# Optimization experiments

Measured on AMD Instinct MI355X. Metric: run time of the kernel, lower is better.

Reference implementation:

```python
import jax, jax.numpy as jnp
import numpy as np

N, C, H, W = 16, 512, 32, 32
NH = 8            # num_heads
HD = C // NH      # head dim c = 64
G = C // 4        # GroupNorm groups = 128
EPS = 1e-5


def conv1x1(X, Wt, b):
    # 1x1 Conv2d == per-pixel linear over channels
    return jnp.einsum('oc,nchw->nohw', Wt, X) + b[None, :, None, None]


def setup_inputs() -> dict:
    key = jax.random.key(0)
    ks = jax.random.split(key, 9)
    s = 0.02
    inp = {
        'X': jax.random.normal(ks[0], (N, C, H, W), jnp.float32),
        'Wq': jax.random.normal(ks[1], (C, C), jnp.float32) * s,
        'bq': jax.random.normal(ks[2], (C,), jnp.float32) * s,
        'Wk': jax.random.normal(ks[3], (C, C), jnp.float32) * s,
        'bk': jax.random.normal(ks[4], (C,), jnp.float32) * s,
        'Wv': jax.random.normal(ks[5], (C, C), jnp.float32) * s,
        'bv': jax.random.normal(ks[6], (C,), jnp.float32) * s,
        'Wo': jax.random.normal(ks[7], (C, C), jnp.float32) * s,
        'bo': jax.random.normal(ks[8], (C,), jnp.float32) * s,
        'gn_w': jnp.ones((C,), jnp.float32),
        'gn_b': jnp.zeros((C,), jnp.float32),
    }
    return inp


def reference(X, Wq, bq, Wk, bk, Wv, bv, Wo, bo, gn_w, gn_b):
    # NOTE: original torch code does  K, Q, V = (Q_conv(X), K_conv(X), V_conv(X))
    # i.e. K gets the Q_conv weights and Q gets the K_conv weights; mirror that.
    K = conv1x1(X, Wq, bq)
    Q = conv1x1(X, Wk, bk)
    V = conv1x1(X, Wv, bv)

    d = H * W
    Kh = K.reshape(N, NH, HD, d)  # [n,h,c,d]
    Qh = Q.reshape(N, NH, HD, d)
    Vh = V.reshape(N, NH, HD, d)

    # softmax-free channel attention: (Q^T K) then V (Q^T K)^T
    A = jnp.einsum('nhcd,nhcD->nhdD', Qh, Kh)   # [n,h,d,d]
    O = jnp.einsum('nhdD,nhcD->nhcd', A, Vh)    # [n,h,c,d]

    O = O.reshape(N, C, H, W)
    O = conv1x1(O, Wo, bo)

    # GroupNorm(G, C) with affine, eps=1e-5
    Og = O.reshape(N, G, C // G, H, W)
    mu = Og.mean(axis=(2, 3, 4), keepdims=True)
    var = Og.var(axis=(2, 3, 4), keepdims=True)
    On = ((Og - mu) * jax.lax.rsqrt(var + EPS)).reshape(N, C, H, W)
    On = On * gn_w[None, :, None, None] + gn_b[None, :, None, None]

    return On + X
```

## Files before the change

### kernel.cpp

```cpp
#include <hip/hip_runtime.h>
#include <hip/hip_bf16.h>

typedef __attribute__((ext_vector_type(8))) short s8v;
typedef __attribute__((ext_vector_type(4))) short s4v;
typedef __attribute__((ext_vector_type(4))) float f32x4;

#define MFMA_BF16 __builtin_amdgcn_mfma_f32_16x16x32_bf16

__device__ inline void gload_lds16(const __hip_bfloat16* g, __hip_bfloat16* l) {
  __builtin_amdgcn_global_load_lds(
      (const __attribute__((address_space(1))) void*)g,
      (__attribute__((address_space(3))) void*)l, 16, 0, 0);
}

__device__ inline short f2bs(float x) {
  __hip_bfloat16 b = __float2bfloat16(x);
  return *reinterpret_cast<short*>(&b);
}

__device__ inline void storeC(float* p, float v) { *p = v; }
__device__ inline void storeC(__hip_bfloat16* p, float v) { *p = __float2bfloat16(v); }

__global__ __launch_bounds__(256) void prep(const float* __restrict__ X,
                                            __hip_bfloat16* __restrict__ XT,
                                            __hip_bfloat16* __restrict__ Xc,
                                            const float* __restrict__ Wq,
                                            const float* __restrict__ Wv,
                                            const float* __restrict__ Wk,
                                            const float* __restrict__ Wo,
                                            const float* __restrict__ bq,
                                            const float* __restrict__ bv,
                                            __hip_bfloat16* __restrict__ WA,
                                            __hip_bfloat16* __restrict__ WkT,
                                            __hip_bfloat16* __restrict__ WOb,
                                            float* __restrict__ biasKV) {
  const int tid = threadIdx.x;
  if (blockIdx.z == 16) {
    const int blk = blockIdx.y * 16 + blockIdx.x;
#pragma unroll
    for (int t = 0; t < 8; ++t) {
      const int i = (blk * 8 + t) * 256 + tid;
      WA[i] = __float2bfloat16(Wq[i]);
      WA[262144 + i] = __float2bfloat16(Wv[i]);
      WOb[i] = __float2bfloat16(Wo[i]);
      WkT[i] = __float2bfloat16(Wk[(i & 511) * 512 + (i >> 9)]);
      if (i < 512) { biasKV[i] = bq[i]; biasKV[512 + i] = bv[i]; }
    }
    return;
  }
  __shared__ float tl[64][65];
  const int n = blockIdx.z;
  const int c0 = blockIdx.y * 64, p0 = blockIdx.x * 64;
  const int lr = tid >> 4, lc4 = (tid & 15) * 4;
  const float* Xp = X + ((long)n * 512 + c0) * 1024 + p0;
  __hip_bfloat16* Xcp = Xc + ((long)n * 512 + c0) * 1024 + p0;
#pragma unroll
  for (int i = 0; i < 4; ++i) {
    const int ch = i * 16 + lr;
    const float4 v = *(const float4*)&Xp[(long)ch * 1024 + lc4];
    tl[ch][lc4 + 0] = v.x; tl[ch][lc4 + 1] = v.y;
    tl[ch][lc4 + 2] = v.z; tl[ch][lc4 + 3] = v.w;
    s4v xo;
    xo[0] = f2bs(v.x); xo[1] = f2bs(v.y); xo[2] = f2bs(v.z); xo[3] = f2bs(v.w);
    *(s4v*)&Xcp[(long)ch * 1024 + lc4] = xo;
  }
  __syncthreads();
  __hip_bfloat16* XTp = XT + ((long)n * 1024 + p0) * 512 + c0;
#pragma unroll
  for (int i = 0; i < 4; ++i) {
    const int px = i * 16 + lr;
    s4v o;
#pragma unroll
    for (int e = 0; e < 4; ++e) o[e] = f2bs(tl[lc4 + e][px]);
    *(s4v*)&XTp[(long)px * 512 + lc4] = o;
  }
}

template <typename OutT, bool BROW>
__global__ __launch_bounds__(256) void gemm_nt(
    const __hip_bfloat16* __restrict__ A, long strideA,
    const __hip_bfloat16* __restrict__ B, long strideB,
    OutT* __restrict__ C, long strideC, int K, int ldc,
    const float* __restrict__ brow, long strideBrow) {
  A += blockIdx.z * strideA;
  B += blockIdx.z * strideB;
  C += blockIdx.z * strideC;
  const int m0 = blockIdx.y * 128;
  const int n0 = blockIdx.x * 128;
  const int tid = threadIdx.x;
  const int wid = tid >> 6, lane = tid & 63;
  const int wm = wid >> 1, wn = wid & 1;

  __shared__ __hip_bfloat16 As[128 * 64];
  __shared__ __hip_bfloat16 Bs[128 * 64];

  f32x4 acc[4][4] = {};

  const __hip_bfloat16* gA0 = A + (long)(m0 + wid * 32 + (lane >> 3)) * K + (lane & 7) * 8;
  const __hip_bfloat16* gB0 = B + (long)(n0 + wid * 32 + (lane >> 3)) * K + (lane & 7) * 8;

  for (int k0 = 0; k0 < K; k0 += 64) {
#pragma unroll
    for (int t = 0; t < 4; ++t) {
      gload_lds16(gA0 + (long)t * 8 * K + k0, &As[(wid * 32 + t * 8) * 64]);
      gload_lds16(gB0 + (long)t * 8 * K + k0, &Bs[(wid * 32 + t * 8) * 64]);
    }
    __syncthreads();
#pragma unroll
    for (int ks = 0; ks < 2; ++ks) {
      const int koff = ks * 32 + (lane >> 4) * 8;
      s8v a[4], b[4];
#pragma unroll
      for (int i = 0; i < 4; ++i)
        a[i] = *(const s8v*)&As[(wm * 64 + i * 16 + (lane & 15)) * 64 + koff];
#pragma unroll
      for (int j = 0; j < 4; ++j)
        b[j] = *(const s8v*)&Bs[(wn * 64 + j * 16 + (lane & 15)) * 64 + koff];
#pragma unroll
      for (int i = 0; i < 4; ++i)
#pragma unroll
        for (int j = 0; j < 4; ++j)
          acc[i][j] = MFMA_BF16(a[i], b[j], acc[i][j], 0, 0, 0);
    }
    __syncthreads();
  }

  const int cr = (lane >> 4) * 4;
  const int cc = lane & 15;
#pragma unroll
  for (int i = 0; i < 4; ++i) {
#pragma unroll
    for (int r = 0; r < 4; ++r) {
      const int gm = m0 + wm * 64 + i * 16 + cr + r;
      const float rb = BROW ? brow[blockIdx.z * strideBrow + gm] : 0.f;
#pragma unroll
      for (int j = 0; j < 4; ++j) {
        const int gn = n0 + wn * 64 + j * 16 + cc;
        storeC(&C[(long)gm * ldc + gn], acc[i][j][r] + rb);
      }
    }
  }
}

__global__ __launch_bounds__(512) void gemm_vkT(const __hip_bfloat16* __restrict__ V,
                                                const __hip_bfloat16* __restrict__ Kk,
                                                __hip_bfloat16* __restrict__ Mt) {
  const int n = blockIdx.x >> 3, h = blockIdx.x & 7;
  const int tid = threadIdx.x, wid = tid >> 6, lane = tid & 63;
  f32x4 acc[4][4] = {};
  const long colbase = (long)n * 1024 + wid * 128 + (lane >> 4) * 8;
  const __hip_bfloat16* Vb = V + (long)(h * 64 + (lane & 15)) * 16384 + colbase;
  const __hip_bfloat16* Kb = Kk + (long)(h * 64 + (lane & 15)) * 16384 + colbase;
#pragma unroll
  for (int kk = 0; kk < 128; kk += 32) {
    s8v a[4], b[4];
#pragma unroll
    for (int i = 0; i < 4; ++i) a[i] = *(const s8v*)(Vb + (long)i * 16 * 16384 + kk);
#pragma unroll
    for (int j = 0; j < 4; ++j) b[j] = *(const s8v*)(Kb + (long)j * 16 * 16384 + kk);
#pragma unroll
    for (int i = 0; i < 4; ++i)
#pragma unroll
      for (int j = 0; j < 4; ++j) acc[i][j] = MFMA_BF16(a[i], b[j], acc[i][j], 0, 0, 0);
  }
  __shared__ float part[4][4096];
  const int cr = (lane >> 4) * 4, cc = lane & 15;
  if (wid < 4) {
#pragma unroll
    for (int i = 0; i < 4; ++i)
#pragma unroll
      for (int r = 0; r < 4; ++r)
#pragma unroll
        for (int j = 0; j < 4; ++j)
          part[wid][(i * 16 + cr + r) * 64 + j * 16 + cc] = acc[i][j][r];
  }
  __syncthreads();
  if (wid >= 4) {
#pragma unroll
    for (int i = 0; i < 4; ++i)
#pragma unroll
      for (int r = 0; r < 4; ++r)
#pragma unroll
        for (int j = 0; j < 4; ++j)
          part[wid - 4][(i * 16 + cr + r) * 64 + j * 16 + cc] += acc[i][j][r];
  }
  __syncthreads();
  __hip_bfloat16* outp = Mt + ((long)n * 8 + h) * 4096;
  for (int e = tid; e < 4096; e += 512) {
    const float sum = part[0][e] + part[1][e] + part[2][e] + part[3][e];
    outp[(e & 63) * 64 + (e >> 6)] = __float2bfloat16(sum);
  }
}

__global__ __launch_bounds__(256) void wchain(const __hip_bfloat16* __restrict__ WOb,
                                              const __hip_bfloat16* __restrict__ WkT,
                                              const __hip_bfloat16* __restrict__ Mt,
                                              const float* __restrict__ bk,
                                              const float* __restrict__ bo,
                                              __hip_bfloat16* __restrict__ WPP,
                                              float* __restrict__ b2out) {
  const int c0 = blockIdx.x * 128, o0 = blockIdx.y * 128, n = blockIdx.z;
  const int tid = threadIdx.x, wid = tid >> 6, lane = tid & 63;
  const int wm = wid >> 1, wn = wid & 1;
  const int cr = (lane >> 4) * 4, cc = lane & 15;

  __shared__ __hip_bfloat16 WoS[128 * 64];
  __shared__ __hip_bfloat16 WkS[128 * 64];
  __shared__ __hip_bfloat16 MtS[64 * 64];
  __shared__ __hip_bfloat16 W1S[128 * 64];
  __shared__ float bkS[512];

  if (tid < 128) *(float4*)&bkS[tid * 4] = *(const float4*)&bk[tid * 4];

  f32x4 acc2[4][4] = {};
  float bacc = 0.f;
  const int r8 = lane >> 3, b8 = (lane & 7) * 8;

  for (int h = 0; h < 8; ++h) {
#pragma unroll
    for (int t = 0; t < 4; ++t) {
      const int row = wid * 32 + t * 8;
      gload_lds16(WOb + (long)(o0 + row + r8) * 512 + h * 64 + b8, &WoS[row * 64]);
      gload_lds16(WkT + (long)(c0 + row + r8) * 512 + h * 64 + b8, &WkS[row * 64]);
    }
    {
      const __hip_bfloat16* mg = Mt + ((long)n * 8 + h) * 4096;
      gload_lds16(mg + wid * 512 + lane * 8, &MtS[wid * 512]);
      gload_lds16(mg + 2048 + wid * 512 + lane * 8, &MtS[2048 + wid * 512]);
    }
    __syncthreads();

    f32x4 acc1[2][4] = {};
#pragma unroll
    for (int ks = 0; ks < 2; ++ks) {
      const int ko = ks * 32 + (lane >> 4) * 8;
      s8v aj[2], bw[4];
#pragma unroll
      for (int i = 0; i < 2; ++i)
        aj[i] = *(const s8v*)&MtS[(wn * 32 + i * 16 + cc) * 64 + ko];
#pragma unroll
      for (int t = 0; t < 4; ++t)
        bw[t] = *(const s8v*)&WoS[(wm * 64 + t * 16 + cc) * 64 + ko];
#pragma unroll
      for (int i = 0; i < 2; ++i)
#pragma unroll
        for (int t = 0; t < 4; ++t)
          acc1[i][t] = MFMA_BF16(aj[i], bw[t], acc1[i][t], 0, 0, 0);
    }
#pragma unroll
    for (int i = 0; i < 2; ++i)
#pragma unroll
      for (int t = 0; t < 4; ++t) {
        const int o = wm * 64 + t * 16 + cc;
        const int jb = wn * 32 + i * 16 + cr;
        s4v p;
#pragma unroll
        for (int r = 0; r < 4; ++r) p[r] = f2bs(acc1[i][t][r]);
        *(s4v*)((char*)W1S + ((o * 128 + jb * 2) ^ ((o & 7) << 4))) = p;
      }
    __syncthreads();

#pragma unroll
    for (int ks = 0; ks < 2; ++ks) {
      const int ko = ks * 32 + (lane >> 4) * 8;
      s8v a2[4], bw[4];
#pragma unroll
      for (int i = 0; i < 4; ++i) {
        const int o = wm * 64 + i * 16 + cc;
        a2[i] = *(const s8v*)((char*)W1S + ((o * 128 + ko * 2) ^ ((o & 7) << 4)));
      }
#pragma unroll
      for (int t = 0; t < 4; ++t)
        bw[t] = *(const s8v*)&WkS[(wn * 64 + t * 16 + cc) * 64 + ko];
#pragma unroll
      for (int i = 0; i < 4; ++i)
#pragma unroll
        for (int t = 0; t < 4; ++t)
          acc2[i][t] = MFMA_BF16(a2[i], bw[t], acc2[i][t], 0, 0, 0);
    }

    if (c0 == 0) {
      const int o = tid >> 1, half = tid & 1;
      float s = 0.f;
#pragma unroll
      for (int q = 0; q < 4; ++q) {
        const int jb = half * 64 + q * 16;
        const s8v w = *(const s8v*)((char*)W1S + ((o * 128 + jb) ^ ((o & 7) << 4)));
        const __hip_bfloat16* wb = (const __hip_bfloat16*)&w;
#pragma unroll
        for (int e = 0; e < 8; ++e)
          s += __bfloat162float(wb[e]) * bkS[h * 64 + half * 32 + q * 8 + e];
      }
      bacc += s;
    }
    __syncthreads();
  }

#pragma unroll
  for (int i = 0; i < 4; ++i)
#pragma unroll
    for (int r = 0; r < 4; ++r)
#pragma unroll
      for (int t = 0; t < 4; ++t)
        WPP[((long)n * 512 + o0 + wm * 64 + i * 16 + cr + r) * 512 +
            c0 + wn * 64 + t * 16 + cc] = __float2bfloat16(acc2[i][t][r]);
  if (c0 == 0) {
    const float tot = bacc + __shfl_xor(bacc, 1);
    if ((tid & 1) == 0) {
      const int o = tid >> 1;
      b2out[n * 512 + o0 + o] = tot + bo[o0 + o];
    }
  }
}

__global__ __launch_bounds__(512) void ygn(const __hip_bfloat16* __restrict__ WPP,
                                           const __hip_bfloat16* __restrict__ XT,
                                           const float* __restrict__ b2,
                                           const __hip_bfloat16* __restrict__ Xc,
                                           const float* __restrict__ gw,
                                           const float* __restrict__ gb,
                                           float* __restrict__ out) {
  const int id = blockIdx.x;
  const int xcd = id & 7, slot = id >> 3;
  const int n = xcd * 2 + (slot >> 4);
  const int ch0 = (slot & 15) * 32;
  const int tid = threadIdx.x, wid = tid >> 6, lane = tid & 63;
  const int wm = wid & 1, wpx = wid >> 1;
  const int cc = lane & 15, cr = (lane >> 4) * 4;

  __shared__ __hip_bfloat16 As[32 * 520];
  __shared__ __hip_bfloat16 Bs[2][256 * 64];
  __shared__ float chS[32][2];
  __shared__ float gS[8][2];

  {
    const __hip_bfloat16* wp = WPP + ((long)n * 512 + ch0) * 512;
    const int row = tid >> 4, e0 = (tid & 15) * 32;
#pragma unroll
    for (int q = 0; q < 4; ++q)
      *(s8v*)&As[row * 520 + e0 + q * 8] =
          *(const s8v*)(wp + (long)row * 512 + e0 + q * 8);
  }
  if (tid < 64) chS[tid >> 1][tid & 1] = 0.f;

  const __hip_bfloat16* xb = XT + (long)n * 1024 * 512;
  const int swz = ((lane & 7) ^ (lane >> 3)) * 8;
  auto STAGE = [&](int it, int buf) {
    const int pcs = it >> 3, kcs = it & 7;
#pragma unroll
    for (int t = 0; t < 4; ++t) {
      const int r0 = wid * 32 + t * 8;
      gload_lds16(xb + (long)(pcs * 256 + r0 + (lane >> 3)) * 512 + kcs * 64 + swz,
                  &Bs[buf][r0 * 64]);
    }
  };

  f32x4 acc[4][4] = {};
  STAGE(0, 0);

#pragma unroll
  for (int pc = 0; pc < 4; ++pc) {
    for (int kc = 0; kc < 8; ++kc) {
      const int it = pc * 8 + kc;
      const int cur = kc & 1;
      asm volatile("s_waitcnt vmcnt(0) lgkmcnt(0)" ::: "memory");
      __builtin_amdgcn_s_barrier();
      __builtin_amdgcn_sched_barrier(0);
      if (it < 31) STAGE(it + 1, cur ^ 1);
#pragma unroll
      for (int ks = 0; ks < 2; ++ks) {
        const int ko = ks * 32 + (lane >> 4) * 8;
        const int g = ks * 4 + (lane >> 4);
        const s8v a = *(const s8v*)&As[(wm * 16 + cc) * 520 + kc * 64 + ko];
#pragma unroll
        for (int j = 0; j < 4; ++j) {
          const int row = wpx * 64 + j * 16 + cc;
          const s8v b = *(const s8v*)((const char*)&Bs[cur][0] +
                                      ((row << 7) | ((g ^ (cc & 7)) << 4)));
          acc[pc][j] = MFMA_BF16(a, b, acc[pc][j], 0, 0, 0);
        }
      }
    }
  }

  float b2v[4], gwv[4], gbv[4];
#pragma unroll
  for (int r = 0; r < 4; ++r) {
    const int ch = ch0 + wm * 16 + cr + r;
    b2v[r] = b2[n * 512 + ch];
    gwv[r] = gw[ch];
    gbv[r] = gb[ch];
  }
  float s[4] = {}, s2[4] = {};
#pragma unroll
  for (int pc = 0; pc < 4; ++pc)
#pragma unroll
    for (int j = 0; j < 4; ++j)
#pragma unroll
      for (int r = 0; r < 4; ++r) {
        const float v = acc[pc][j][r] + b2v[r];
        acc[pc][j][r] = v;
        s[r] += v;
        s2[r] += v * v;
      }
#pragma unroll
  for (int off = 1; off < 16; off <<= 1)
#pragma unroll
    for (int r = 0; r < 4; ++r) {
      s[r] += __shfl_xor(s[r], off);
      s2[r] += __shfl_xor(s2[r], off);
    }
  __syncthreads();
  if (cc == 0) {
#pragma unroll
    for (int r = 0; r < 4; ++r) {
      atomicAdd(&chS[wm * 16 + cr + r][0], s[r]);
      atomicAdd(&chS[wm * 16 + cr + r][1], s2[r]);
    }
  }
  __syncthreads();
  if (tid < 8) {
    const int g = tid;
    float ts = 0.f, t2 = 0.f;
#pragma unroll
    for (int c = 0; c < 4; ++c) { ts += chS[g * 4 + c][0]; t2 += chS[g * 4 + c][1]; }
    const float mu = ts * (1.f / 4096.f);
    const float var = t2 * (1.f / 4096.f) - mu * mu;
    gS[g][0] = mu;
    gS[g][1] = rsqrtf(var + 1e-5f);
  }
  __syncthreads();

#pragma unroll
  for (int r = 0; r < 4; ++r) {
    const int chl = wm * 16 + cr + r;
    const int ch = ch0 + chl;
    const float mu = gS[chl >> 2][0], rstd = gS[chl >> 2][1];
    const float sc = rstd * gwv[r], sh = gbv[r];
    float* op = out + ((long)n * 512 + ch) * 1024;
    const __hip_bfloat16* xr = Xc + ((long)n * 512 + ch) * 1024;
#pragma unroll
    for (int pc = 0; pc < 4; ++pc)
#pragma unroll
      for (int j = 0; j < 4; ++j) {
        const int px = pc * 256 + wpx * 64 + j * 16 + cc;
        op[px] = (acc[pc][j][r] - mu) * sc + sh + __bfloat162float(xr[px]);
      }
  }
}

extern "C" void kernel_launch(void* const* d_in, const int* in_sizes, int n_in,
                              void* d_out, int out_size, void* d_ws, size_t ws_size,
                              hipStream_t stream) {
  const float* X  = (const float*)d_in[0];
  const float* Wq = (const float*)d_in[1];
  const float* bq = (const float*)d_in[2];
  const float* Wk = (const float*)d_in[3];
  const float* bk = (const float*)d_in[4];
  const float* Wv = (const float*)d_in[5];
  const float* bv = (const float*)d_in[6];
  const float* Wo = (const float*)d_in[7];
  const float* bo = (const float*)d_in[8];
  const float* gw = (const float*)d_in[9];
  const float* gb = (const float*)d_in[10];
  float* out = (float*)d_out;

  char* ws = (char*)d_ws;
  __hip_bfloat16* XT  = (__hip_bfloat16*)(ws + 0);
  __hip_bfloat16* KV  = (__hip_bfloat16*)(ws + 16777216);
  __hip_bfloat16* WPP = (__hip_bfloat16*)(ws + 58720256);
  __hip_bfloat16* Mt  = (__hip_bfloat16*)(ws + 67108864);
  __hip_bfloat16* WA  = (__hip_bfloat16*)(ws + 68157440);
  __hip_bfloat16* WkT = (__hip_bfloat16*)(ws + 69206016);
  __hip_bfloat16* WOb = (__hip_bfloat16*)(ws + 69730304);
  float*          bKV = (float*)(ws + 70254592);
  float*          b2  = (float*)(ws + 70258688);
  __hip_bfloat16* Xc  = (__hip_bfloat16*)(ws + 75497472);

  prep<<<dim3(16, 8, 17), 256, 0, stream>>>(X, XT, Xc, Wq, Wv, Wk, Wo, bq, bv,
                                            WA, WkT, WOb, bKV);
  gemm_nt<__hip_bfloat16, true><<<dim3(128, 8, 1), 256, 0, stream>>>(
      WA, 0, XT, 0, KV, 0, 512, 16384, bKV, 0);
  gemm_vkT<<<128, 512, 0, stream>>>(KV + (long)512 * 16384, KV, Mt);
  wchain<<<dim3(4, 4, 16), 256, 0, stream>>>(WOb, WkT, Mt, bk, bo, WPP, b2);
  ygn<<<256, 512, 0, stream>>>(WPP, XT, b2, Xc, gw, gb, out);
}
```

Measured before the change: 118.7 us.

## Fuse K/V projection with per-head V·Kᵀ reduction into one kernel

Replaces the separate K/V projection GEMM (which wrote a bf16 KV buffer to global memory) and the V·Kᵀ kernel with one kernel. Each block computes K and V for a 128-pixel slice of one head, keeps them in LDS, and writes a partial 64x64 fp32 product. wchain then sums the 8 partials per (n,h) when it loads Mt. This avoids the round trip of the large KV intermediate and one launch. In exchange it adds fp32 partial traffic and redundant partial summation in every wchain block.

```diff
diff --git a/kernel.cpp b/kernel.cpp
--- a/kernel.cpp
+++ b/kernel.cpp
@@ -17,9 +17,6 @@
   __hip_bfloat16 b = __float2bfloat16(x);
   return *reinterpret_cast<short*>(&b);
 }
-
-__device__ inline void storeC(float* p, float v) { *p = v; }
-__device__ inline void storeC(__hip_bfloat16* p, float v) { *p = __float2bfloat16(v); }
 
 __global__ __launch_bounds__(256) void prep(const float* __restrict__ X,
                                             __hip_bfloat16* __restrict__ XT,
@@ -76,125 +73,123 @@
   }
 }
 
-template <typename OutT, bool BROW>
-__global__ __launch_bounds__(256) void gemm_nt(
-    const __hip_bfloat16* __restrict__ A, long strideA,
-    const __hip_bfloat16* __restrict__ B, long strideB,
-    OutT* __restrict__ C, long strideC, int K, int ldc,
-    const float* __restrict__ brow, long strideBrow) {
-  A += blockIdx.z * strideA;
-  B += blockIdx.z * strideB;
-  C += blockIdx.z * strideC;
-  const int m0 = blockIdx.y * 128;
-  const int n0 = blockIdx.x * 128;
-  const int tid = threadIdx.x;
-  const int wid = tid >> 6, lane = tid & 63;
+__global__ __launch_bounds__(256) void kvm(const __hip_bfloat16* __restrict__ WA,
+                                           const __hip_bfloat16* __restrict__ XT,
+                                           const float* __restrict__ bKV,
+                                           float* __restrict__ Part) {
+  const int b = blockIdx.x;
+  const int n = b >> 6, h = (b >> 3) & 7, t = b & 7;
+  const int tid = threadIdx.x, wid = tid >> 6, lane = tid & 63;
   const int wm = wid >> 1, wn = wid & 1;
-
-  __shared__ __hip_bfloat16 As[128 * 64];
-  __shared__ __hip_bfloat16 Bs[128 * 64];
-
-  f32x4 acc[4][4] = {};
-
-  const __hip_bfloat16* gA0 = A + (long)(m0 + wid * 32 + (lane >> 3)) * K + (lane & 7) * 8;
-  const __hip_bfloat16* gB0 = B + (long)(n0 + wid * 32 + (lane >> 3)) * K + (lane & 7) * 8;
-
-  for (int k0 = 0; k0 < K; k0 += 64) {
-#pragma unroll
-    for (int t = 0; t < 4; ++t) {
-      gload_lds16(gA0 + (long)t * 8 * K + k0, &As[(wid * 32 + t * 8) * 64]);
-      gload_lds16(gB0 + (long)t * 8 * K + k0, &Bs[(wid * 32 + t * 8) * 64]);
-    }
+  const int cr = (lane >> 4) * 4, cc = lane & 15;
+
+  __shared__ __hip_bfloat16 KS[64 * 136];
+  __shared__ __hip_bfloat16 VS[64 * 136];
+  __shared__ float part2[2][4096];
+  __hip_bfloat16* AqS = (__hip_bfloat16*)&part2[0][0];
+  __hip_bfloat16* AvS = AqS + 64 * 64;
+  __hip_bfloat16* BS  = AvS + 64 * 64;
+
+  f32x4 aK[2][4] = {}, aV[2][4] = {};
+
+  const int r8 = lane >> 3, b8 = (lane & 7) * 8;
+  const __hip_bfloat16* gq = WA + (long)(h * 64 + wid * 16 + r8) * 512 + b8;
+  const __hip_bfloat16* gv = gq + (long)512 * 512;
+  const __hip_bfloat16* gx = XT + (long)(n * 1024 + t * 128 + wid * 32 + r8) * 512 + b8;
+
+  for (int k0 = 0; k0 < 512; k0 += 64) {
+#pragma unroll
+    for (int u = 0; u < 2; ++u) {
+      gload_lds16(gq + (long)(u * 8) * 512 + k0, &AqS[(wid * 16 + u * 8) * 64]);
+      gload_lds16(gv + (long)(u * 8) * 512 + k0, &AvS[(wid * 16 + u * 8) * 64]);
+    }
+#pragma unroll
+    for (int u = 0; u < 4; ++u)
+      gload_lds16(gx + (long)(u * 8) * 512 + k0, &BS[(wid * 32 + u * 8) * 64]);
     __syncthreads();
 #pragma unroll
     for (int ks = 0; ks < 2; ++ks) {
-      const int koff = ks * 32 + (lane >> 4) * 8;
-      s8v a[4], b[4];
-#pragma unroll
-      for (int i = 0; i < 4; ++i)
-        a[i] = *(const s8v*)&As[(wm * 64 + i * 16 + (lane & 15)) * 64 + koff];
+      const int ko = ks * 32 + (lane >> 4) * 8;
+      s8v q[2], v[2], bb[4];
+#pragma unroll
+      for (int i = 0; i < 2; ++i) {
+        q[i] = *(const s8v*)&AqS[(wm * 32 + i * 16 + cc) * 64 + ko];
+        v[i] = *(const s8v*)&AvS[(wm * 32 + i * 16 + cc) * 64 + ko];
+      }
 #pragma unroll
       for (int j = 0; j < 4; ++j)
-        b[j] = *(const s8v*)&Bs[(wn * 64 + j * 16 + (lane & 15)) * 64 + koff];
-#pragma unroll
-      for (int i = 0; i < 4; ++i)
+        bb[j] = *(const s8v*)&BS[(wn * 64 + j * 16 + cc) * 64 + ko];
+#pragma unroll
+      for (int i = 0; i < 2; ++i)
+#pragma unroll
+        for (int j = 0; j < 4; ++j) {
+          aK[i][j] = MFMA_BF16(q[i], bb[j], aK[i][j], 0, 0, 0);
+          aV[i][j] = MFMA_BF16(v[i], bb[j], aV[i][j], 0, 0, 0);
+        }
+    }
+    __syncthreads();
+  }
+
+#pragma unroll
+  for (int i = 0; i < 2; ++i)
+#pragma unroll
+    for (int r = 0; r < 4; ++r) {
+      const int ch = wm * 32 + i * 16 + cr + r;
+      const float bk_ = bKV[h * 64 + ch];
+      const float bv_ = bKV[512 + h * 64 + ch];
+#pragma unroll
+      for (int j = 0; j < 4; ++j) {
+        const int px = wn * 64 + j * 16 + cc;
+        KS[ch * 136 + px] = __float2bfloat16(aK[i][j][r] + bk_);
+        VS[ch * 136 + px] = __float2bfloat16(aV[i][j][r] + bv_);
+      }
+    }
+  __syncthreads();
+
+  f32x4 m[4][4] = {};
+  {
+    const int pxb = wid * 32 + (lane >> 4) * 8;
+    s8v av[4], ak[4];
+#pragma unroll
+    for (int i = 0; i < 4; ++i)
+      av[i] = *(const s8v*)&VS[((lane & 15) + i * 16) * 136 + pxb];
+#pragma unroll
+    for (int j = 0; j < 4; ++j)
+      ak[j] = *(const s8v*)&KS[((lane & 15) + j * 16) * 136 + pxb];
+#pragma unroll
+    for (int i = 0; i < 4; ++i)
+#pragma unroll
+      for (int j = 0; j < 4; ++j)
+        m[i][j] = MFMA_BF16(av[i], ak[j], m[i][j], 0, 0, 0);
+  }
+  if (wid < 2) {
+#pragma unroll
+    for (int i = 0; i < 4; ++i)
+#pragma unroll
+      for (int r = 0; r < 4; ++r)
 #pragma unroll
         for (int j = 0; j < 4; ++j)
-          acc[i][j] = MFMA_BF16(a[i], b[j], acc[i][j], 0, 0, 0);
-    }
-    __syncthreads();
-  }
-
-  const int cr = (lane >> 4) * 4;
-  const int cc = lane & 15;
-#pragma unroll
-  for (int i = 0; i < 4; ++i) {
-#pragma unroll
-    for (int r = 0; r < 4; ++r) {
-      const int gm = m0 + wm * 64 + i * 16 + cr + r;
-      const float rb = BROW ? brow[blockIdx.z * strideBrow + gm] : 0.f;
-#pragma unroll
-      for (int j = 0; j < 4; ++j) {
-        const int gn = n0 + wn * 64 + j * 16 + cc;
-        storeC(&C[(long)gm * ldc + gn], acc[i][j][r] + rb);
-      }
-    }
-  }
-}
-
-__global__ __launch_bounds__(512) void gemm_vkT(const __hip_bfloat16* __restrict__ V,
-                                                const __hip_bfloat16* __restrict__ Kk,
-                                                __hip_bfloat16* __restrict__ Mt) {
-  const int n = blockIdx.x >> 3, h = blockIdx.x & 7;
-  const int tid = threadIdx.x, wid = tid >> 6, lane = tid & 63;
-  f32x4 acc[4][4] = {};
-  const long colbase = (long)n * 1024 + wid * 128 + (lane >> 4) * 8;
-  const __hip_bfloat16* Vb = V + (long)(h * 64 + (lane & 15)) * 16384 + colbase;
-  const __hip_bfloat16* Kb = Kk + (long)(h * 64 + (lane & 15)) * 16384 + colbase;
-#pragma unroll
-  for (int kk = 0; kk < 128; kk += 32) {
-    s8v a[4], b[4];
-#pragma unroll
-    for (int i = 0; i < 4; ++i) a[i] = *(const s8v*)(Vb + (long)i * 16 * 16384 + kk);
-#pragma unroll
-    for (int j = 0; j < 4; ++j) b[j] = *(const s8v*)(Kb + (long)j * 16 * 16384 + kk);
+          part2[wid][(i * 16 + cr + r) * 64 + j * 16 + cc] = m[i][j][r];
+  }
+  __syncthreads();
+  if (wid >= 2) {
 #pragma unroll
     for (int i = 0; i < 4; ++i)
 #pragma unroll
-      for (int j = 0; j < 4; ++j) acc[i][j] = MFMA_BF16(a[i], b[j], acc[i][j], 0, 0, 0);
-  }
-  __shared__ float part[4][4096];
-  const int cr = (lane >> 4) * 4, cc = lane & 15;
-  if (wid < 4) {
-#pragma unroll
-    for (int i = 0; i < 4; ++i)
-#pragma unroll
       for (int r = 0; r < 4; ++r)
 #pragma unroll
         for (int j = 0; j < 4; ++j)
-          part[wid][(i * 16 + cr + r) * 64 + j * 16 + cc] = acc[i][j][r];
-  }
-  __syncthreads();
-  if (wid >= 4) {
-#pragma unroll
-    for (int i = 0; i < 4; ++i)
-#pragma unroll
-      for (int r = 0; r < 4; ++r)
-#pragma unroll
-        for (int j = 0; j < 4; ++j)
-          part[wid - 4][(i * 16 + cr + r) * 64 + j * 16 + cc] += acc[i][j][r];
-  }
-  __syncthreads();
-  __hip_bfloat16* outp = Mt + ((long)n * 8 + h) * 4096;
-  for (int e = tid; e < 4096; e += 512) {
-    const float sum = part[0][e] + part[1][e] + part[2][e] + part[3][e];
-    outp[(e & 63) * 64 + (e >> 6)] = __float2bfloat16(sum);
-  }
+          part2[wid - 2][(i * 16 + cr + r) * 64 + j * 16 + cc] += m[i][j][r];
+  }
+  __syncthreads();
+  float* outp = Part + (long)b * 4096;
+  for (int e = tid; e < 4096; e += 256)
+    outp[(e & 63) * 64 + (e >> 6)] = part2[0][e] + part2[1][e];
 }
 
 __global__ __launch_bounds__(256) void wchain(const __hip_bfloat16* __restrict__ WOb,
                                               const __hip_bfloat16* __restrict__ WkT,
-                                              const __hip_bfloat16* __restrict__ Mt,
+                                              const float* __restrict__ Part,
                                               const float* __restrict__ bk,
                                               const float* __restrict__ bo,
                                               __hip_bfloat16* __restrict__ WPP,
@@ -224,9 +219,20 @@
       gload_lds16(WkT + (long)(c0 + row + r8) * 512 + h * 64 + b8, &WkS[row * 64]);
     }
     {
-      const __hip_bfloat16* mg = Mt + ((long)n * 8 + h) * 4096;
-      gload_lds16(mg + wid * 512 + lane * 8, &MtS[wid * 512]);
-      gload_lds16(mg + 2048 + wid * 512 + lane * 8, &MtS[2048 + wid * 512]);
+      const float* P0 = Part + ((long)((n * 8 + h) * 8)) * 4096;
+#pragma unroll
+      for (int q = 0; q < 4; ++q) {
+        const int e = tid * 16 + q * 4;
+        float4 s = *(const float4*)&P0[e];
+#pragma unroll
+        for (int p = 1; p < 8; ++p) {
+          const float4 x = *(const float4*)&P0[(long)p * 4096 + e];
+          s.x += x.x; s.y += x.y; s.z += x.z; s.w += x.w;
+        }
+        s4v o;
+        o[0] = f2bs(s.x); o[1] = f2bs(s.y); o[2] = f2bs(s.z); o[3] = f2bs(s.w);
+        *(s4v*)&MtS[e] = o;
+      }
     }
     __syncthreads();
 
@@ -467,9 +473,8 @@
 
   char* ws = (char*)d_ws;
   __hip_bfloat16* XT  = (__hip_bfloat16*)(ws + 0);
-  __hip_bfloat16* KV  = (__hip_bfloat16*)(ws + 16777216);
+  float*          Part= (float*)(ws + 16777216);
   __hip_bfloat16* WPP = (__hip_bfloat16*)(ws + 58720256);
-  __hip_bfloat16* Mt  = (__hip_bfloat16*)(ws + 67108864);
   __hip_bfloat16* WA  = (__hip_bfloat16*)(ws + 68157440);
   __hip_bfloat16* WkT = (__hip_bfloat16*)(ws + 69206016);
   __hip_bfloat16* WOb = (__hip_bfloat16*)(ws + 69730304);
@@ -479,9 +484,7 @@
 
   prep<<<dim3(16, 8, 17), 256, 0, stream>>>(X, XT, Xc, Wq, Wv, Wk, Wo, bq, bv,
                                             WA, WkT, WOb, bKV);
-  gemm_nt<__hip_bfloat16, true><<<dim3(128, 8, 1), 256, 0, stream>>>(
-      WA, 0, XT, 0, KV, 0, 512, 16384, bKV, 0);
-  gemm_vkT<<<128, 512, 0, stream>>>(KV + (long)512 * 16384, KV, Mt);
-  wchain<<<dim3(4, 4, 16), 256, 0, stream>>>(WOb, WkT, Mt, bk, bo, WPP, b2);
+  kvm<<<1024, 256, 0, stream>>>(WA, XT, bKV, Part);
+  wchain<<<dim3(4, 4, 16), 256, 0, stream>>>(WOb, WkT, Part, bk, bo, WPP, b2);
   ygn<<<256, 512, 0, stream>>>(WPP, XT, b2, Xc, gw, gb, out);
 }
```

New measurement: 147.6 us. 24.3% more time.
